# Performance work log

Hardware: AMD Instinct MI355X
Metric: run time of the kernel (lower is better)

The kernel has to match this reference:

```python
import jax, jax.numpy as jnp
import numpy as np
import math

B, S, D, H = 2, 2048, 1024, 16
DK = D // H


def setup_inputs() -> dict:
    key = jax.random.key(0)
    ks = jax.random.split(key, 11)
    f = jnp.float32
    return {
        "query": jax.random.normal(ks[0], (B, S, D), f),
        "key": jax.random.normal(ks[1], (B, S, D), f),
        "value": jax.random.normal(ks[2], (B, S, D), f),
        "wq": jax.random.normal(ks[3], (D, D), f) * 0.02,
        "bq": jnp.zeros((D,), f),
        "wk": jax.random.normal(ks[4], (D, D), f) * 0.02,
        "bk": jnp.zeros((D,), f),
        "wv": jax.random.normal(ks[5], (D, D), f) * 0.02,
        "bv": jnp.zeros((D,), f),
        "wo": jax.random.normal(ks[6], (D, D), f) * 0.02,
        "bo": jnp.zeros((D,), f),
    }


def reference(query, key, value, wq, bq, wk, bk, wv, bv, wo, bo):
    # Linear projections (torch Linear: y = x @ W.T + b)
    q = query @ wq.T + bq
    k = key @ wk.T + bk
    v = value @ wv.T + bv
    # [B,S,D] -> [B,H,S,DK]
    q = q.reshape(B, S, H, DK).transpose(0, 2, 1, 3)
    k = k.reshape(B, S, H, DK).transpose(0, 2, 1, 3)
    v = v.reshape(B, S, H, DK).transpose(0, 2, 1, 3)
    scores = jnp.einsum("bhqd,bhkd->bhqk", q, k) / math.sqrt(DK)
    causal = jnp.triu(jnp.ones((S, S), dtype=bool), k=1)  # strict upper triangle masked
    scores = jnp.where(causal, -jnp.inf, scores)
    attn = jax.nn.softmax(scores, axis=-1)  # dropout is identity in eval (p=0)
    x = jnp.einsum("bhqk,bhkd->bhqd", attn, v)
    x = x.transpose(0, 2, 1, 3).reshape(B, S, D)
    return x @ wo.T + bo
```

## Files before the change

### kernel.cpp

```cpp
#include <hip/hip_runtime.h>
#include <math.h>

#define BB 2
#define SS 2048
#define DD 1024
#define HH 16
#define DKK 64
#define MM (BB * SS)
#define KK DD
#define VSTR 2176

typedef __attribute__((ext_vector_type(8))) short short8;
typedef __attribute__((ext_vector_type(4))) float floatx4;

__device__ inline unsigned short f2bf(float x) {
    unsigned int u = __float_as_uint(x);
    u += 0x7fffu + ((u >> 16) & 1u);
    return (unsigned short)(u >> 16);
}

__device__ inline unsigned int pkbf(float a, float b) {
    return (__float_as_uint(b) & 0xffff0000u) | (__float_as_uint(a) >> 16);
}

__device__ inline void cast4f(const float* __restrict__ in, unsigned short* __restrict__ out, int i) {
    const float4 v = *(const float4*)(in + i);
    unsigned long long pk = (unsigned long long)f2bf(v.x)
                          | ((unsigned long long)f2bf(v.y) << 16)
                          | ((unsigned long long)f2bf(v.z) << 32)
                          | ((unsigned long long)f2bf(v.w) << 48);
    *(unsigned long long*)(out + i) = pk;
}

__global__ __launch_bounds__(256) void cast_all(const float* __restrict__ q, const float* __restrict__ k,
                                                const float* __restrict__ v,
                                                const float* __restrict__ wq, const float* __restrict__ wk,
                                                const float* __restrict__ wv, const float* __restrict__ wo,
                                                unsigned short* __restrict__ oq, unsigned short* __restrict__ ok,
                                                unsigned short* __restrict__ ov,
                                                unsigned short* __restrict__ owq, unsigned short* __restrict__ owk,
                                                unsigned short* __restrict__ owv, unsigned short* __restrict__ owo) {
    const int tid = blockIdx.x * 256 + threadIdx.x;
    #pragma unroll
    for (int it = 0; it < 8; ++it) {
        const int g = tid + it * 524288;
        const float* in;
        unsigned short* out;
        int idx;
        if (g < 3145728) {
            const int w = g >> 20;
            idx = g & 1048575;
            in  = (w == 0) ? q : (w == 1) ? k : v;
            out = (w == 0) ? oq : (w == 1) ? ok : ov;
        } else {
            const int gw = g - 3145728;
            const int w = gw >> 18;
            idx = gw & 262143;
            in  = (w == 0) ? wq : (w == 1) ? wk : (w == 2) ? wv : wo;
            out = (w == 0) ? owq : (w == 1) ? owk : (w == 2) ? owv : owo;
        }
        cast4f(in, out, idx * 4);
    }
}

#define GLDS(gp, lp) __builtin_amdgcn_global_load_lds( \
    (const __attribute__((address_space(1))) void*)(gp), \
    (__attribute__((address_space(3))) void*)(lp), 16, 0, 0)

#define SCHED0() __builtin_amdgcn_sched_barrier(0)
#define BAR()    __builtin_amdgcn_s_barrier()
#define WAITL0() asm volatile("s_waitcnt lgkmcnt(0)" ::: "memory")
#define WAITV(n) asm volatile("s_waitcnt vmcnt(" #n ")" ::: "memory")

__device__ __forceinline__ void gemm128_body(const unsigned short* __restrict__ A,
                                             const unsigned short* __restrict__ W,
                                             int m0, int n0,
                                             unsigned short* __restrict__ As,
                                             unsigned short* __restrict__ Bs,
                                             floatx4 (&acc)[4][4]) {
    const int t    = threadIdx.x;
    const int lane = t & 63;
    const int wave = t >> 6;
    const int col  = lane & 15;
    const int quad = lane >> 4;
    const int wm   = (wave >> 1) * 64;
    const int wn   = (wave & 1) * 64;

    const int r  = t >> 3;
    const int cs = t & 7;

    const int sA0 = (quad ^ (col & 7)) * 8;
    const int sA1 = ((quad + 4) ^ (col & 7)) * 8;

    auto stage = [&](int kt, int pb) {
        const int k0 = kt * 64;
        #pragma unroll
        for (int g = 0; g < 4; ++g) {
            const int row = g * 32 + r;
            const int ksw = (cs ^ (row & 7)) * 8;
            GLDS(A + (size_t)(m0 + row) * KK + k0 + ksw,
                 &As[pb * (128 * 64) + row * 64 + cs * 8]);
        }
        #pragma unroll
        for (int g = 0; g < 4; ++g) {
            const int row = g * 32 + r;
            const int ksw = (cs ^ (row & 7)) * 8;
            GLDS(W + (size_t)(n0 + row) * KK + k0 + ksw,
                 &Bs[pb * (128 * 64) + row * 64 + cs * 8]);
        }
    };

    stage(0, 0);
    WAITV(0); SCHED0(); BAR(); SCHED0();

    const int NK = KK / 64;
    for (int kt = 0; kt < NK; ++kt) {
        const int p = kt & 1;
        if (kt + 1 < NK) stage(kt + 1, p ^ 1);

        const unsigned short* Ab = &As[p * (128 * 64)];
        const unsigned short* Bb = &Bs[p * (128 * 64)];
        short8 a0[4], a1[4], b0[4], b1[4];
        #pragma unroll
        for (int i = 0; i < 4; ++i) {
            const unsigned short* ar = Ab + (wm + i * 16 + col) * 64;
            a0[i] = *(const short8*)(ar + sA0);
            a1[i] = *(const short8*)(ar + sA1);
        }
        #pragma unroll
        for (int j = 0; j < 4; ++j) {
            const unsigned short* br = Bb + (wn + j * 16 + col) * 64;
            b0[j] = *(const short8*)(br + sA0);
            b1[j] = *(const short8*)(br + sA1);
        }

        __builtin_amdgcn_s_setprio(1);
        #pragma unroll
        for (int i = 0; i < 4; ++i)
            #pragma unroll
            for (int j = 0; j < 4; ++j)
                acc[i][j] = __builtin_amdgcn_mfma_f32_16x16x32_bf16(a0[i], b0[j], acc[i][j], 0, 0, 0);
        #pragma unroll
        for (int i = 0; i < 4; ++i)
            #pragma unroll
            for (int j = 0; j < 4; ++j)
                acc[i][j] = __builtin_amdgcn_mfma_f32_16x16x32_bf16(a1[i], b1[j], acc[i][j], 0, 0, 0);
        __builtin_amdgcn_s_setprio(0);

        WAITL0(); SCHED0();
        if (kt + 1 < NK) { WAITV(0); }
        SCHED0(); BAR(); SCHED0();
    }
}

__global__ __launch_bounds__(256, 2) void gemm_qkv(const unsigned short* __restrict__ qB,
                                                   const unsigned short* __restrict__ kB,
                                                   const unsigned short* __restrict__ vB,
                                                   const unsigned short* __restrict__ wqB,
                                                   const unsigned short* __restrict__ wkB,
                                                   const unsigned short* __restrict__ wvB,
                                                   const float* __restrict__ bq,
                                                   const float* __restrict__ bk,
                                                   const float* __restrict__ bv,
                                                   unsigned short* __restrict__ Qh,
                                                   unsigned short* __restrict__ Kh,
                                                   unsigned short* __restrict__ Vt) {
    __shared__ __align__(16) unsigned short As[2 * 128 * 64];
    __shared__ __align__(16) unsigned short Bs[2 * 128 * 64];

    const int bid   = blockIdx.x;
    const int wgid  = (bid & 7) * 96 + (bid >> 3);
    const int which = wgid >> 8;
    const int tile  = wgid & 255;
    const int m0    = (tile >> 3) * 128;
    const int n0    = (tile & 7) * 128;

    const unsigned short* A = (which == 0) ? qB : (which == 1) ? kB : vB;
    const unsigned short* W = (which == 0) ? wqB : (which == 1) ? wkB : wvB;
    const float* bias       = (which == 0) ? bq : (which == 1) ? bk : bv;

    floatx4 acc[4][4] = {};
    gemm128_body(A, W, m0, n0, As, Bs, acc);

    const int t    = threadIdx.x;
    const int lane = t & 63;
    const int wave = t >> 6;
    const int col  = lane & 15;
    const int quad = lane >> 4;
    const int wm   = (wave >> 1) * 64;
    const int wn   = (wave & 1) * 64;

    #pragma unroll
    for (int i = 0; i < 4; ++i) {
        #pragma unroll
        for (int j = 0; j < 4; ++j) {
            const int n  = n0 + wn + j * 16 + col;
            const float bv0 = bias[n];
            const int h = n >> 6, dk = n & 63;
            const int mb  = m0 + wm + i * 16 + quad * 4;
            const int bdx = mb >> 11, s = mb & 2047;
            if (which != 2) {
                unsigned short* O = (which == 0) ? Qh : Kh;
                #pragma unroll
                for (int rr = 0; rr < 4; ++rr)
                    O[(((size_t)(bdx * HH + h)) * SS + (s + rr)) * DKK + dk] = f2bf(acc[i][j][rr] + bv0);
            } else {
                unsigned short* vp = Vt + (((size_t)(bdx * HH + h)) * DKK + dk) * VSTR + s;
                uint2 w;
                w.x = (unsigned int)f2bf(acc[i][j][0] + bv0) | ((unsigned int)f2bf(acc[i][j][1] + bv0) << 16);
                w.y = (unsigned int)f2bf(acc[i][j][2] + bv0) | ((unsigned int)f2bf(acc[i][j][3] + bv0) << 16);
                *(uint2*)vp = w;
            }
        }
    }
}

__global__ __launch_bounds__(256, 2) void gemm_out(const unsigned short* __restrict__ A,
                                                   const unsigned short* __restrict__ W,
                                                   const float* __restrict__ bias,
                                                   float* __restrict__ C) {
    __shared__ __align__(16) unsigned short As[2 * 128 * 64];
    __shared__ __align__(16) unsigned short Bs[2 * 128 * 64];

    const int bid  = blockIdx.x;
    const int wgid = (bid & 7) * 32 + (bid >> 3);
    const int m0   = (wgid >> 3) * 128;
    const int n0   = (wgid & 7) * 128;

    floatx4 acc[4][4] = {};
    gemm128_body(A, W, m0, n0, As, Bs, acc);

    const int t    = threadIdx.x;
    const int lane = t & 63;
    const int wave = t >> 6;
    const int col  = lane & 15;
    const int quad = lane >> 4;
    const int wm   = (wave >> 1) * 64;
    const int wn   = (wave & 1) * 64;

    #pragma unroll
    for (int i = 0; i < 4; ++i) {
        #pragma unroll
        for (int j = 0; j < 4; ++j) {
            const int n = n0 + wn + j * 16 + col;
            const float bv0 = bias[n];
            #pragma unroll
            for (int rr = 0; rr < 4; ++rr) {
                const int m = m0 + wm + i * 16 + quad * 4 + rr;
                C[(size_t)m * DD + n] = acc[i][j][rr] + bv0;
            }
        }
    }
}

#define C1 0.18033688011112042f
#define C2 11.541560327111707f
#define MFMA __builtin_amdgcn_mfma_f32_16x16x32_bf16

__global__ __launch_bounds__(512) void attn_mfma(const unsigned short* __restrict__ Qh,
                                                 const unsigned short* __restrict__ Kh,
                                                 const unsigned short* __restrict__ Vt,
                                                 unsigned short* __restrict__ X) {
    __shared__ __align__(16) unsigned short Ks[2][64 * 64];
    __shared__ __align__(16) unsigned short Vs[2][64 * 64];
    __shared__ __align__(16) unsigned short Plds[8][16 * 40];

    const int t    = threadIdx.x;
    const int lane = t & 63;
    const int wave = t >> 6;
    const int col  = lane & 15;
    const int quad = lane >> 4;

    const int lin = blockIdx.x;
    const int bh  = (lin & 7) + 8 * ((lin >> 3) & 3);
    const int pr  = lin >> 5;
    const int b   = bh / HH, h = bh % HH;

    const int cX  = (wave < 4) ? (31 - pr) : pr;
    const int q0  = cX * 64 + (wave & 3) * 16;
    const int nst = 32 - pr;

    const unsigned short* Kb = Kh + (size_t)bh * SS * DKK;
    const unsigned short* Vb = Vt + (size_t)bh * DKK * VSTR;

    const int r0  = t >> 3;
    const int sg0 = ((t & 7) ^ (r0 & 7)) * 8;

    unsigned short* Pw = &Plds[wave][0];

    const unsigned short* Qb = Qh + ((size_t)bh * SS + q0) * DKK;
    const short8 qa0 = *(const short8*)(Qb + (size_t)col * DKK + quad * 8);
    const short8 qa1 = *(const short8*)(Qb + (size_t)col * DKK + 32 + quad * 8);

    floatx4 o0 = {0.f, 0.f, 0.f, 0.f}, o1 = o0, o2 = o0, o3 = o0;
    float lp = 0.f;

    const int ksA = ((quad)      ^ (col & 7)) * 8;
    const int ksB = ((quad | 4)  ^ (col & 7)) * 8;

    GLDS(Kb + (size_t)r0 * DKK + sg0,  &Ks[0][t * 8]);
    GLDS(Vb + (size_t)r0 * VSTR + sg0, &Vs[0][t * 8]);

    int cur = 0;
    for (int kb = 0; kb < nst; ++kb) {
        __syncthreads();

        if (kb + 1 < nst) {
            const int jn = (kb + 1) * 64;
            const int nx = cur ^ 1;
            GLDS(Kb + (size_t)(jn + r0) * DKK + sg0,  &Ks[nx][t * 8]);
            GLDS(Vb + (size_t)r0 * VSTR + jn + sg0,   &Vs[nx][t * 8]);
        }

        const unsigned short* Kp = &Ks[cur][0];
        const unsigned short* Vp = &Vs[cur][0];

        #pragma unroll
        for (int hh = 0; hh < 2; ++hh) {
            const int j0 = kb * 64 + hh * 32;
            if (j0 < q0 + 16) {
                const short8 k0 = *(const short8*)(Kp + (hh * 32 + col) * 64 + ksA);
                const short8 k1 = *(const short8*)(Kp + (hh * 32 + col) * 64 + ksB);
                const short8 k2 = *(const short8*)(Kp + (hh * 32 + col + 16) * 64 + ksA);
                const short8 k3 = *(const short8*)(Kp + (hh * 32 + col + 16) * 64 + ksB);

                floatx4 t0 = {0.f, 0.f, 0.f, 0.f}, t1 = t0;
                __builtin_amdgcn_s_setprio(1);
                t0 = MFMA(k0, qa0, t0, 0, 0, 0);
                t0 = MFMA(k1, qa1, t0, 0, 0, 0);
                t1 = MFMA(k2, qa0, t1, 0, 0, 0);
                t1 = MFMA(k3, qa1, t1, 0, 0, 0);
                __builtin_amdgcn_s_setprio(0);

                float p[8];
                if (j0 + 31 > q0) {
                    const int lim = q0 + col - j0;
                    #pragma unroll
                    for (int r = 0; r < 4; ++r) {
                        p[r]     = (quad * 4 + r      <= lim) ? __builtin_exp2f(fmaf(t0[r], C1, -C2)) : 0.f;
                        p[4 + r] = (16 + quad * 4 + r <= lim) ? __builtin_exp2f(fmaf(t1[r], C1, -C2)) : 0.f;
                    }
                } else {
                    #pragma unroll
                    for (int r = 0; r < 4; ++r) {
                        p[r]     = __builtin_exp2f(fmaf(t0[r], C1, -C2));
                        p[4 + r] = __builtin_exp2f(fmaf(t1[r], C1, -C2));
                    }
                }
                lp += (p[0] + p[1]) + (p[2] + p[3]) + (p[4] + p[5]) + (p[6] + p[7]);

                uint2 w0 = { pkbf(p[0], p[1]), pkbf(p[2], p[3]) };
                uint2 w1 = { pkbf(p[4], p[5]), pkbf(p[6], p[7]) };
                *(uint2*)(Pw + col * 40 + quad * 4)      = w0;
                *(uint2*)(Pw + col * 40 + 16 + quad * 4) = w1;

                const short8 pb = *(const short8*)(Pw + col * 40 + quad * 8);
                const int vs = hh ? ksB : ksA;
                const short8 v0 = *(const short8*)(Vp + (col)      * 64 + vs);
                const short8 v1 = *(const short8*)(Vp + (col + 16) * 64 + vs);
                const short8 v2 = *(const short8*)(Vp + (col + 32) * 64 + vs);
                const short8 v3 = *(const short8*)(Vp + (col + 48) * 64 + vs);
                __builtin_amdgcn_s_setprio(1);
                o0 = MFMA(v0, pb, o0, 0, 0, 0);
                o1 = MFMA(v1, pb, o1, 0, 0, 0);
                o2 = MFMA(v2, pb, o2, 0, 0, 0);
                o3 = MFMA(v3, pb, o3, 0, 0, 0);
                __builtin_amdgcn_s_setprio(0);
            }
        }

        cur ^= 1;
    }

    lp += __shfl_xor(lp, 16, 64);
    lp += __shfl_xor(lp, 32, 64);
    const float li = 1.f / lp;

    unsigned short* Xp = X + ((size_t)(b * SS + q0 + col)) * DD + h * DKK + quad * 4;
    {
        uint2 w;
        w.x = (unsigned int)f2bf(o0[0] * li) | ((unsigned int)f2bf(o0[1] * li) << 16);
        w.y = (unsigned int)f2bf(o0[2] * li) | ((unsigned int)f2bf(o0[3] * li) << 16);
        *(uint2*)(Xp + 0) = w;
        w.x = (unsigned int)f2bf(o1[0] * li) | ((unsigned int)f2bf(o1[1] * li) << 16);
        w.y = (unsigned int)f2bf(o1[2] * li) | ((unsigned int)f2bf(o1[3] * li) << 16);
        *(uint2*)(Xp + 16) = w;
        w.x = (unsigned int)f2bf(o2[0] * li) | ((unsigned int)f2bf(o2[1] * li) << 16);
        w.y = (unsigned int)f2bf(o2[2] * li) | ((unsigned int)f2bf(o2[3] * li) << 16);
        *(uint2*)(Xp + 32) = w;
        w.x = (unsigned int)f2bf(o3[0] * li) | ((unsigned int)f2bf(o3[1] * li) << 16);
        w.y = (unsigned int)f2bf(o3[2] * li) | ((unsigned int)f2bf(o3[3] * li) << 16);
        *(uint2*)(Xp + 48) = w;
    }
}

extern "C" void kernel_launch(void* const* d_in, const int* in_sizes, int n_in,
                              void* d_out, int out_size, void* d_ws, size_t ws_size,
                              hipStream_t stream) {
    const float* query = (const float*)d_in[0];
    const float* key   = (const float*)d_in[1];
    const float* value = (const float*)d_in[2];
    const float* wq    = (const float*)d_in[3];
    const float* bq    = (const float*)d_in[4];
    const float* wk    = (const float*)d_in[5];
    const float* bk    = (const float*)d_in[6];
    const float* wv    = (const float*)d_in[7];
    const float* bv    = (const float*)d_in[8];
    const float* wo    = (const float*)d_in[9];
    const float* bo    = (const float*)d_in[10];

    char* ws = (char*)d_ws;
    const size_t MB = 1024 * 1024;
    unsigned short* qB  = (unsigned short*)(ws);
    unsigned short* kB  = (unsigned short*)(ws + 8 * MB);
    unsigned short* vB  = (unsigned short*)(ws + 16 * MB);
    unsigned short* wqB = (unsigned short*)(ws + 24 * MB);
    unsigned short* wkB = (unsigned short*)(ws + 26 * MB);
    unsigned short* wvB = (unsigned short*)(ws + 28 * MB);
    unsigned short* woB = (unsigned short*)(ws + 30 * MB);
    unsigned short* Qh  = (unsigned short*)(ws + 32 * MB);
    unsigned short* Kh  = (unsigned short*)(ws + 40 * MB);
    unsigned short* Vt  = (unsigned short*)(ws + 48 * MB);
    unsigned short* Xb  = qB;

    cast_all<<<2048, 256, 0, stream>>>(query, key, value, wq, wk, wv, wo,
                                       qB, kB, vB, wqB, wkB, wvB, woB);

    gemm_qkv<<<768, 256, 0, stream>>>(qB, kB, vB, wqB, wkB, wvB, bq, bk, bv, Qh, Kh, Vt);

    attn_mfma<<<512, 512, 0, stream>>>(Qh, Kh, Vt, Xb);

    gemm_out<<<256, 256, 0, stream>>>(Xb, woB, bo, (float*)d_out);
}
```

Before: 219.8 us.

## Fuse fp32-to-bf16 casts into GEMM tile loading, drop separate cast kernel

```diff
diff --git a/kernel.cpp b/kernel.cpp
--- a/kernel.cpp
+++ b/kernel.cpp
@@ -23,44 +23,19 @@
     return (__float_as_uint(b) & 0xffff0000u) | (__float_as_uint(a) >> 16);
 }
 
-__device__ inline void cast4f(const float* __restrict__ in, unsigned short* __restrict__ out, int i) {
-    const float4 v = *(const float4*)(in + i);
-    unsigned long long pk = (unsigned long long)f2bf(v.x)
-                          | ((unsigned long long)f2bf(v.y) << 16)
-                          | ((unsigned long long)f2bf(v.z) << 32)
-                          | ((unsigned long long)f2bf(v.w) << 48);
-    *(unsigned long long*)(out + i) = pk;
-}
-
-__global__ __launch_bounds__(256) void cast_all(const float* __restrict__ q, const float* __restrict__ k,
-                                                const float* __restrict__ v,
-                                                const float* __restrict__ wq, const float* __restrict__ wk,
-                                                const float* __restrict__ wv, const float* __restrict__ wo,
-                                                unsigned short* __restrict__ oq, unsigned short* __restrict__ ok,
-                                                unsigned short* __restrict__ ov,
-                                                unsigned short* __restrict__ owq, unsigned short* __restrict__ owk,
-                                                unsigned short* __restrict__ owv, unsigned short* __restrict__ owo) {
-    const int tid = blockIdx.x * 256 + threadIdx.x;
-    #pragma unroll
-    for (int it = 0; it < 8; ++it) {
-        const int g = tid + it * 524288;
-        const float* in;
-        unsigned short* out;
-        int idx;
-        if (g < 3145728) {
-            const int w = g >> 20;
-            idx = g & 1048575;
-            in  = (w == 0) ? q : (w == 1) ? k : v;
-            out = (w == 0) ? oq : (w == 1) ? ok : ov;
-        } else {
-            const int gw = g - 3145728;
-            const int w = gw >> 18;
-            idx = gw & 262143;
-            in  = (w == 0) ? wq : (w == 1) ? wk : (w == 2) ? wv : wo;
-            out = (w == 0) ? owq : (w == 1) ? owk : (w == 2) ? owv : owo;
-        }
-        cast4f(in, out, idx * 4);
-    }
+__device__ inline unsigned int rhu2(float a, float b) {
+    const unsigned int au = __float_as_uint(a) + 0x8000u;
+    const unsigned int bu = __float_as_uint(b) + 0x8000u;
+    return (bu & 0xffff0000u) | (au >> 16);
+}
+
+__device__ inline short8 pack8(const float4 x, const float4 y) {
+    union { unsigned int u[4]; short8 s; } r;
+    r.u[0] = rhu2(x.x, x.y);
+    r.u[1] = rhu2(x.z, x.w);
+    r.u[2] = rhu2(y.x, y.y);
+    r.u[3] = rhu2(y.z, y.w);
+    return r.s;
 }
 
 #define GLDS(gp, lp) __builtin_amdgcn_global_load_lds( \
@@ -72,93 +47,13 @@
 #define WAITL0() asm volatile("s_waitcnt lgkmcnt(0)" ::: "memory")
 #define WAITV(n) asm volatile("s_waitcnt vmcnt(" #n ")" ::: "memory")
 
-__device__ __forceinline__ void gemm128_body(const unsigned short* __restrict__ A,
-                                             const unsigned short* __restrict__ W,
-                                             int m0, int n0,
-                                             unsigned short* __restrict__ As,
-                                             unsigned short* __restrict__ Bs,
-                                             floatx4 (&acc)[4][4]) {
-    const int t    = threadIdx.x;
-    const int lane = t & 63;
-    const int wave = t >> 6;
-    const int col  = lane & 15;
-    const int quad = lane >> 4;
-    const int wm   = (wave >> 1) * 64;
-    const int wn   = (wave & 1) * 64;
-
-    const int r  = t >> 3;
-    const int cs = t & 7;
-
-    const int sA0 = (quad ^ (col & 7)) * 8;
-    const int sA1 = ((quad + 4) ^ (col & 7)) * 8;
-
-    auto stage = [&](int kt, int pb) {
-        const int k0 = kt * 64;
-        #pragma unroll
-        for (int g = 0; g < 4; ++g) {
-            const int row = g * 32 + r;
-            const int ksw = (cs ^ (row & 7)) * 8;
-            GLDS(A + (size_t)(m0 + row) * KK + k0 + ksw,
-                 &As[pb * (128 * 64) + row * 64 + cs * 8]);
-        }
-        #pragma unroll
-        for (int g = 0; g < 4; ++g) {
-            const int row = g * 32 + r;
-            const int ksw = (cs ^ (row & 7)) * 8;
-            GLDS(W + (size_t)(n0 + row) * KK + k0 + ksw,
-                 &Bs[pb * (128 * 64) + row * 64 + cs * 8]);
-        }
-    };
-
-    stage(0, 0);
-    WAITV(0); SCHED0(); BAR(); SCHED0();
-
-    const int NK = KK / 64;
-    for (int kt = 0; kt < NK; ++kt) {
-        const int p = kt & 1;
-        if (kt + 1 < NK) stage(kt + 1, p ^ 1);
-
-        const unsigned short* Ab = &As[p * (128 * 64)];
-        const unsigned short* Bb = &Bs[p * (128 * 64)];
-        short8 a0[4], a1[4], b0[4], b1[4];
-        #pragma unroll
-        for (int i = 0; i < 4; ++i) {
-            const unsigned short* ar = Ab + (wm + i * 16 + col) * 64;
-            a0[i] = *(const short8*)(ar + sA0);
-            a1[i] = *(const short8*)(ar + sA1);
-        }
-        #pragma unroll
-        for (int j = 0; j < 4; ++j) {
-            const unsigned short* br = Bb + (wn + j * 16 + col) * 64;
-            b0[j] = *(const short8*)(br + sA0);
-            b1[j] = *(const short8*)(br + sA1);
-        }
-
-        __builtin_amdgcn_s_setprio(1);
-        #pragma unroll
-        for (int i = 0; i < 4; ++i)
-            #pragma unroll
-            for (int j = 0; j < 4; ++j)
-                acc[i][j] = __builtin_amdgcn_mfma_f32_16x16x32_bf16(a0[i], b0[j], acc[i][j], 0, 0, 0);
-        #pragma unroll
-        for (int i = 0; i < 4; ++i)
-            #pragma unroll
-            for (int j = 0; j < 4; ++j)
-                acc[i][j] = __builtin_amdgcn_mfma_f32_16x16x32_bf16(a1[i], b1[j], acc[i][j], 0, 0, 0);
-        __builtin_amdgcn_s_setprio(0);
-
-        WAITL0(); SCHED0();
-        if (kt + 1 < NK) { WAITV(0); }
-        SCHED0(); BAR(); SCHED0();
-    }
-}
-
-__global__ __launch_bounds__(256, 2) void gemm_qkv(const unsigned short* __restrict__ qB,
-                                                   const unsigned short* __restrict__ kB,
-                                                   const unsigned short* __restrict__ vB,
-                                                   const unsigned short* __restrict__ wqB,
-                                                   const unsigned short* __restrict__ wkB,
-                                                   const unsigned short* __restrict__ wvB,
+
+__global__ __launch_bounds__(256, 2) void gemm_qkv(const float* __restrict__ q,
+                                                   const float* __restrict__ k,
+                                                   const float* __restrict__ v,
+                                                   const float* __restrict__ wq,
+                                                   const float* __restrict__ wk,
+                                                   const float* __restrict__ wv,
                                                    const float* __restrict__ bq,
                                                    const float* __restrict__ bk,
                                                    const float* __restrict__ bv,
@@ -175,12 +70,9 @@
     const int m0    = (tile >> 3) * 128;
     const int n0    = (tile & 7) * 128;
 
-    const unsigned short* A = (which == 0) ? qB : (which == 1) ? kB : vB;
-    const unsigned short* W = (which == 0) ? wqB : (which == 1) ? wkB : wvB;
-    const float* bias       = (which == 0) ? bq : (which == 1) ? bk : bv;
-
-    floatx4 acc[4][4] = {};
-    gemm128_body(A, W, m0, n0, As, Bs, acc);
+    const float* A    = (which == 0) ? q : (which == 1) ? k : v;
+    const float* W    = (which == 0) ? wq : (which == 1) ? wk : wv;
+    const float* bias = (which == 0) ? bq : (which == 1) ? bk : bv;
 
     const int t    = threadIdx.x;
     const int lane = t & 63;
@@ -189,6 +81,86 @@
     const int quad = lane >> 4;
     const int wm   = (wave >> 1) * 64;
     const int wn   = (wave & 1) * 64;
+
+    const int sr = t >> 1;
+    const int kh = t & 1;
+    const float* Ag = A + (size_t)(m0 + sr) * KK + kh * 32;
+    const float* Wg = W + (size_t)(n0 + sr) * KK + kh * 32;
+    int wof[4];
+    #pragma unroll
+    for (int j = 0; j < 4; ++j) wof[j] = sr * 64 + ((kh * 4 + j) ^ (sr & 7)) * 8;
+
+    const int sA0 = (quad ^ (col & 7)) * 8;
+    const int sA1 = ((quad + 4) ^ (col & 7)) * 8;
+
+    floatx4 acc[4][4] = {};
+    float4 la[8], lb[8];
+
+    #pragma unroll
+    for (int i = 0; i < 8; ++i) la[i] = *(const float4*)(Ag + i * 4);
+    #pragma unroll
+    for (int i = 0; i < 8; ++i) lb[i] = *(const float4*)(Wg + i * 4);
+    #pragma unroll
+    for (int j = 0; j < 4; ++j) *(short8*)(&As[wof[j]]) = pack8(la[2 * j], la[2 * j + 1]);
+    #pragma unroll
+    for (int j = 0; j < 4; ++j) *(short8*)(&Bs[wof[j]]) = pack8(lb[2 * j], lb[2 * j + 1]);
+    WAITL0(); SCHED0(); BAR(); SCHED0();
+
+    const int NK = KK / 64;
+    for (int kt = 0; kt < NK; ++kt) {
+        const int p = kt & 1;
+
+        if (kt + 1 < NK) {
+            const float* pa = Ag + (kt + 1) * 64;
+            const float* pw = Wg + (kt + 1) * 64;
+            #pragma unroll
+            for (int i = 0; i < 8; ++i) la[i] = *(const float4*)(pa + i * 4);
+            #pragma unroll
+            for (int i = 0; i < 8; ++i) lb[i] = *(const float4*)(pw + i * 4);
+        }
+        SCHED0();
+
+        const unsigned short* Ab = &As[p * (128 * 64)];
+        const unsigned short* Bb = &Bs[p * (128 * 64)];
+        short8 a0[4], a1[4], b0[4], b1[4];
+        #pragma unroll
+        for (int i = 0; i < 4; ++i) {
+            const unsigned short* ar = Ab + (wm + i * 16 + col) * 64;
+            a0[i] = *(const short8*)(ar + sA0);
+            a1[i] = *(const short8*)(ar + sA1);
+        }
+        #pragma unroll
+        for (int j = 0; j < 4; ++j) {
+            const unsigned short* br = Bb + (wn + j * 16 + col) * 64;
+            b0[j] = *(const short8*)(br + sA0);
+            b1[j] = *(const short8*)(br + sA1);
+        }
+
+        __builtin_amdgcn_s_setprio(1);
+        #pragma unroll
+        for (int i = 0; i < 4; ++i)
+            #pragma unroll
+            for (int j = 0; j < 4; ++j)
+                acc[i][j] = __builtin_amdgcn_mfma_f32_16x16x32_bf16(a0[i], b0[j], acc[i][j], 0, 0, 0);
+        #pragma unroll
+        for (int i = 0; i < 4; ++i)
+            #pragma unroll
+            for (int j = 0; j < 4; ++j)
+                acc[i][j] = __builtin_amdgcn_mfma_f32_16x16x32_bf16(a1[i], b1[j], acc[i][j], 0, 0, 0);
+        __builtin_amdgcn_s_setprio(0);
+
+        if (kt + 1 < NK) {
+            unsigned short* Ad = &As[(p ^ 1) * (128 * 64)];
+            unsigned short* Bd = &Bs[(p ^ 1) * (128 * 64)];
+            #pragma unroll
+            for (int j = 0; j < 4; ++j) *(short8*)(Ad + wof[j]) = pack8(la[2 * j], la[2 * j + 1]);
+            #pragma unroll
+            for (int j = 0; j < 4; ++j) *(short8*)(Bd + wof[j]) = pack8(lb[2 * j], lb[2 * j + 1]);
+        }
+
+        WAITL0(); SCHED0();
+        BAR(); SCHED0();
+    }
 
     #pragma unroll
     for (int i = 0; i < 4; ++i) {
@@ -216,7 +188,7 @@
 }
 
 __global__ __launch_bounds__(256, 2) void gemm_out(const unsigned short* __restrict__ A,
-                                                   const unsigned short* __restrict__ W,
+                                                   const float* __restrict__ W,
                                                    const float* __restrict__ bias,
                                                    float* __restrict__ C) {
     __shared__ __align__(16) unsigned short As[2 * 128 * 64];
@@ -226,9 +198,6 @@
     const int wgid = (bid & 7) * 32 + (bid >> 3);
     const int m0   = (wgid >> 3) * 128;
     const int n0   = (wgid & 7) * 128;
-
-    floatx4 acc[4][4] = {};
-    gemm128_body(A, W, m0, n0, As, Bs, acc);
 
     const int t    = threadIdx.x;
     const int lane = t & 63;
@@ -238,6 +207,92 @@
     const int wm   = (wave >> 1) * 64;
     const int wn   = (wave & 1) * 64;
 
+    const int r  = t >> 3;
+    const int cs = t & 7;
+
+    const int sr = t >> 1;
+    const int kh = t & 1;
+    const float* Wg = W + (size_t)(n0 + sr) * KK + kh * 32;
+    int wof[4];
+    #pragma unroll
+    for (int j = 0; j < 4; ++j) wof[j] = sr * 64 + ((kh * 4 + j) ^ (sr & 7)) * 8;
+
+    const int sA0 = (quad ^ (col & 7)) * 8;
+    const int sA1 = ((quad + 4) ^ (col & 7)) * 8;
+
+    auto stageA = [&](int kt, int pb) {
+        const int k0 = kt * 64;
+        #pragma unroll
+        for (int g = 0; g < 4; ++g) {
+            const int row = g * 32 + r;
+            const int ksw = (cs ^ (row & 7)) * 8;
+            GLDS(A + (size_t)(m0 + row) * KK + k0 + ksw,
+                 &As[pb * (128 * 64) + row * 64 + cs * 8]);
+        }
+    };
+
+    floatx4 acc[4][4] = {};
+    float4 lb[8];
+
+    stageA(0, 0);
+    #pragma unroll
+    for (int i = 0; i < 8; ++i) lb[i] = *(const float4*)(Wg + i * 4);
+    #pragma unroll
+    for (int j = 0; j < 4; ++j) *(short8*)(&Bs[wof[j]]) = pack8(lb[2 * j], lb[2 * j + 1]);
+    WAITL0(); WAITV(0); SCHED0(); BAR(); SCHED0();
+
+    const int NK = KK / 64;
+    for (int kt = 0; kt < NK; ++kt) {
+        const int p = kt & 1;
+
+        if (kt + 1 < NK) {
+            stageA(kt + 1, p ^ 1);
+            const float* pw = Wg + (kt + 1) * 64;
+            #pragma unroll
+            for (int i = 0; i < 8; ++i) lb[i] = *(const float4*)(pw + i * 4);
+        }
+        SCHED0();
+
+        const unsigned short* Ab = &As[p * (128 * 64)];
+        const unsigned short* Bb = &Bs[p * (128 * 64)];
+        short8 a0[4], a1[4], b0[4], b1[4];
+        #pragma unroll
+        for (int i = 0; i < 4; ++i) {
+            const unsigned short* ar = Ab + (wm + i * 16 + col) * 64;
+            a0[i] = *(const short8*)(ar + sA0);
+            a1[i] = *(const short8*)(ar + sA1);
+        }
+        #pragma unroll
+        for (int j = 0; j < 4; ++j) {
+            const unsigned short* br = Bb + (wn + j * 16 + col) * 64;
+            b0[j] = *(const short8*)(br + sA0);
+            b1[j] = *(const short8*)(br + sA1);
+        }
+
+        __builtin_amdgcn_s_setprio(1);
+        #pragma unroll
+        for (int i = 0; i < 4; ++i)
+            #pragma unroll
+            for (int j = 0; j < 4; ++j)
+                acc[i][j] = __builtin_amdgcn_mfma_f32_16x16x32_bf16(a0[i], b0[j], acc[i][j], 0, 0, 0);
+        #pragma unroll
+        for (int i = 0; i < 4; ++i)
+            #pragma unroll
+            for (int j = 0; j < 4; ++j)
+                acc[i][j] = __builtin_amdgcn_mfma_f32_16x16x32_bf16(a1[i], b1[j], acc[i][j], 0, 0, 0);
+        __builtin_amdgcn_s_setprio(0);
+
+        if (kt + 1 < NK) {
+            unsigned short* Bd = &Bs[(p ^ 1) * (128 * 64)];
+            #pragma unroll
+            for (int j = 0; j < 4; ++j) *(short8*)(Bd + wof[j]) = pack8(lb[2 * j], lb[2 * j + 1]);
+        }
+
+        WAITL0(); SCHED0();
+        if (kt + 1 < NK) { WAITV(0); }
+        SCHED0(); BAR(); SCHED0();
+    }
+
     #pragma unroll
     for (int i = 0; i < 4; ++i) {
         #pragma unroll
@@ -336,15 +391,15 @@
                 if (j0 + 31 > q0) {
                     const int lim = q0 + col - j0;
                     #pragma unroll
-                    for (int r = 0; r < 4; ++r) {
-                        p[r]     = (quad * 4 + r      <= lim) ? __builtin_exp2f(fmaf(t0[r], C1, -C2)) : 0.f;
-                        p[4 + r] = (16 + quad * 4 + r <= lim) ? __builtin_exp2f(fmaf(t1[r], C1, -C2)) : 0.f;
+                    for (int rr = 0; rr < 4; ++rr) {
+                        p[rr]     = (quad * 4 + rr      <= lim) ? __builtin_exp2f(fmaf(t0[rr], C1, -C2)) : 0.f;
+                        p[4 + rr] = (16 + quad * 4 + rr <= lim) ? __builtin_exp2f(fmaf(t1[rr], C1, -C2)) : 0.f;
                     }
                 } else {
                     #pragma unroll
-                    for (int r = 0; r < 4; ++r) {
-                        p[r]     = __builtin_exp2f(fmaf(t0[r], C1, -C2));
-                        p[4 + r] = __builtin_exp2f(fmaf(t1[r], C1, -C2));
+                    for (int rr = 0; rr < 4; ++rr) {
+                        p[rr]     = __builtin_exp2f(fmaf(t0[rr], C1, -C2));
+                        p[4 + rr] = __builtin_exp2f(fmaf(t1[rr], C1, -C2));
                     }
                 }
                 lp += (p[0] + p[1]) + (p[2] + p[3]) + (p[4] + p[5]) + (p[6] + p[7]);
@@ -411,24 +466,14 @@
 
     char* ws = (char*)d_ws;
     const size_t MB = 1024 * 1024;
-    unsigned short* qB  = (unsigned short*)(ws);
-    unsigned short* kB  = (unsigned short*)(ws + 8 * MB);
-    unsigned short* vB  = (unsigned short*)(ws + 16 * MB);
-    unsigned short* wqB = (unsigned short*)(ws + 24 * MB);
-    unsigned short* wkB = (unsigned short*)(ws + 26 * MB);
-    unsigned short* wvB = (unsigned short*)(ws + 28 * MB);
-    unsigned short* woB = (unsigned short*)(ws + 30 * MB);
-    unsigned short* Qh  = (unsigned short*)(ws + 32 * MB);
-    unsigned short* Kh  = (unsigned short*)(ws + 40 * MB);
-    unsigned short* Vt  = (unsigned short*)(ws + 48 * MB);
-    unsigned short* Xb  = qB;
-
-    cast_all<<<2048, 256, 0, stream>>>(query, key, value, wq, wk, wv, wo,
-                                       qB, kB, vB, wqB, wkB, wvB, woB);
-
-    gemm_qkv<<<768, 256, 0, stream>>>(qB, kB, vB, wqB, wkB, wvB, bq, bk, bv, Qh, Kh, Vt);
+    unsigned short* Qh = (unsigned short*)(ws);
+    unsigned short* Kh = (unsigned short*)(ws + 8 * MB);
+    unsigned short* Vt = (unsigned short*)(ws + 16 * MB);
+    unsigned short* Xb = (unsigned short*)(ws + 25 * MB);
+
+    gemm_qkv<<<768, 256, 0, stream>>>(query, key, value, wq, wk, wv, bq, bk, bv, Qh, Kh, Vt);
 
     attn_mfma<<<512, 512, 0, stream>>>(Qh, Kh, Vt, Xb);
 
-    gemm_out<<<256, 256, 0, stream>>>(Xb, woB, bo, (float*)d_out);
-}
+    gemm_out<<<256, 256, 0, stream>>>(Xb, wo, bo, (float*)d_out);
+}
```

New measurement: 295.6 us. 1.34x slower.

## Fuse cast, QKV GEMM, attention and output GEMM into one persistent kernel

Applied to the files above, without the earlier changes.

```diff
diff --git a/kernel.cpp b/kernel.cpp
--- a/kernel.cpp
+++ b/kernel.cpp
@@ -9,6 +9,7 @@
 #define MM (BB * SS)
 #define KK DD
 #define VSTR 2176
+#define NBLK 256
 
 typedef __attribute__((ext_vector_type(8))) short short8;
 typedef __attribute__((ext_vector_type(4))) float floatx4;
@@ -32,37 +33,6 @@
     *(unsigned long long*)(out + i) = pk;
 }
 
-__global__ __launch_bounds__(256) void cast_all(const float* __restrict__ q, const float* __restrict__ k,
-                                                const float* __restrict__ v,
-                                                const float* __restrict__ wq, const float* __restrict__ wk,
-                                                const float* __restrict__ wv, const float* __restrict__ wo,
-                                                unsigned short* __restrict__ oq, unsigned short* __restrict__ ok,
-                                                unsigned short* __restrict__ ov,
-                                                unsigned short* __restrict__ owq, unsigned short* __restrict__ owk,
-                                                unsigned short* __restrict__ owv, unsigned short* __restrict__ owo) {
-    const int tid = blockIdx.x * 256 + threadIdx.x;
-    #pragma unroll
-    for (int it = 0; it < 8; ++it) {
-        const int g = tid + it * 524288;
-        const float* in;
-        unsigned short* out;
-        int idx;
-        if (g < 3145728) {
-            const int w = g >> 20;
-            idx = g & 1048575;
-            in  = (w == 0) ? q : (w == 1) ? k : v;
-            out = (w == 0) ? oq : (w == 1) ? ok : ov;
-        } else {
-            const int gw = g - 3145728;
-            const int w = gw >> 18;
-            idx = gw & 262143;
-            in  = (w == 0) ? wq : (w == 1) ? wk : (w == 2) ? wv : wo;
-            out = (w == 0) ? owq : (w == 1) ? owk : (w == 2) ? owv : owo;
-        }
-        cast4f(in, out, idx * 4);
-    }
-}
-
 #define GLDS(gp, lp) __builtin_amdgcn_global_load_lds( \
     (const __attribute__((address_space(1))) void*)(gp), \
     (__attribute__((address_space(3))) void*)(lp), 16, 0, 0)
@@ -72,19 +42,31 @@
 #define WAITL0() asm volatile("s_waitcnt lgkmcnt(0)" ::: "memory")
 #define WAITV(n) asm volatile("s_waitcnt vmcnt(" #n ")" ::: "memory")
 
-__device__ __forceinline__ void gemm128_body(const unsigned short* __restrict__ A,
+__device__ inline void grid_sync(unsigned int* bar) {
+    __syncthreads();
+    if (threadIdx.x == 0) {
+        __threadfence();
+        const unsigned a = atomicAdd(&bar[0], 1u);
+        const unsigned target = ((a >> 8) + 1u) << 8;
+        while (atomicAdd(&bar[0], 0u) < target) __builtin_amdgcn_s_sleep(8);
+        __threadfence();
+    }
+    __syncthreads();
+}
+
+__device__ __forceinline__ void gemm512_body(const unsigned short* __restrict__ A,
                                              const unsigned short* __restrict__ W,
                                              int m0, int n0,
                                              unsigned short* __restrict__ As,
                                              unsigned short* __restrict__ Bs,
-                                             floatx4 (&acc)[4][4]) {
+                                             floatx4 (&acc)[4][2]) {
     const int t    = threadIdx.x;
     const int lane = t & 63;
     const int wave = t >> 6;
     const int col  = lane & 15;
     const int quad = lane >> 4;
-    const int wm   = (wave >> 1) * 64;
-    const int wn   = (wave & 1) * 64;
+    const int wm   = (wave >> 2) * 64;
+    const int wn   = (wave & 3) * 32;
 
     const int r  = t >> 3;
     const int cs = t & 7;
@@ -95,15 +77,15 @@
     auto stage = [&](int kt, int pb) {
         const int k0 = kt * 64;
         #pragma unroll
-        for (int g = 0; g < 4; ++g) {
-            const int row = g * 32 + r;
+        for (int g = 0; g < 2; ++g) {
+            const int row = g * 64 + r;
             const int ksw = (cs ^ (row & 7)) * 8;
             GLDS(A + (size_t)(m0 + row) * KK + k0 + ksw,
                  &As[pb * (128 * 64) + row * 64 + cs * 8]);
         }
         #pragma unroll
-        for (int g = 0; g < 4; ++g) {
-            const int row = g * 32 + r;
+        for (int g = 0; g < 2; ++g) {
+            const int row = g * 64 + r;
             const int ksw = (cs ^ (row & 7)) * 8;
             GLDS(W + (size_t)(n0 + row) * KK + k0 + ksw,
                  &Bs[pb * (128 * 64) + row * 64 + cs * 8]);
@@ -120,7 +102,7 @@
 
         const unsigned short* Ab = &As[p * (128 * 64)];
         const unsigned short* Bb = &Bs[p * (128 * 64)];
-        short8 a0[4], a1[4], b0[4], b1[4];
+        short8 a0[4], a1[4], b0[2], b1[2];
         #pragma unroll
         for (int i = 0; i < 4; ++i) {
             const unsigned short* ar = Ab + (wm + i * 16 + col) * 64;
@@ -128,7 +110,7 @@
             a1[i] = *(const short8*)(ar + sA1);
         }
         #pragma unroll
-        for (int j = 0; j < 4; ++j) {
+        for (int j = 0; j < 2; ++j) {
             const unsigned short* br = Bb + (wn + j * 16 + col) * 64;
             b0[j] = *(const short8*)(br + sA0);
             b1[j] = *(const short8*)(br + sA1);
@@ -138,12 +120,12 @@
         #pragma unroll
         for (int i = 0; i < 4; ++i)
             #pragma unroll
-            for (int j = 0; j < 4; ++j)
+            for (int j = 0; j < 2; ++j)
                 acc[i][j] = __builtin_amdgcn_mfma_f32_16x16x32_bf16(a0[i], b0[j], acc[i][j], 0, 0, 0);
         #pragma unroll
         for (int i = 0; i < 4; ++i)
             #pragma unroll
-            for (int j = 0; j < 4; ++j)
+            for (int j = 0; j < 2; ++j)
                 acc[i][j] = __builtin_amdgcn_mfma_f32_16x16x32_bf16(a1[i], b1[j], acc[i][j], 0, 0, 0);
         __builtin_amdgcn_s_setprio(0);
 
@@ -153,125 +135,25 @@
     }
 }
 
-__global__ __launch_bounds__(256, 2) void gemm_qkv(const unsigned short* __restrict__ qB,
-                                                   const unsigned short* __restrict__ kB,
-                                                   const unsigned short* __restrict__ vB,
-                                                   const unsigned short* __restrict__ wqB,
-                                                   const unsigned short* __restrict__ wkB,
-                                                   const unsigned short* __restrict__ wvB,
-                                                   const float* __restrict__ bq,
-                                                   const float* __restrict__ bk,
-                                                   const float* __restrict__ bv,
-                                                   unsigned short* __restrict__ Qh,
-                                                   unsigned short* __restrict__ Kh,
-                                                   unsigned short* __restrict__ Vt) {
-    __shared__ __align__(16) unsigned short As[2 * 128 * 64];
-    __shared__ __align__(16) unsigned short Bs[2 * 128 * 64];
-
-    const int bid   = blockIdx.x;
-    const int wgid  = (bid & 7) * 96 + (bid >> 3);
-    const int which = wgid >> 8;
-    const int tile  = wgid & 255;
-    const int m0    = (tile >> 3) * 128;
-    const int n0    = (tile & 7) * 128;
-
-    const unsigned short* A = (which == 0) ? qB : (which == 1) ? kB : vB;
-    const unsigned short* W = (which == 0) ? wqB : (which == 1) ? wkB : wvB;
-    const float* bias       = (which == 0) ? bq : (which == 1) ? bk : bv;
-
-    floatx4 acc[4][4] = {};
-    gemm128_body(A, W, m0, n0, As, Bs, acc);
-
+#define C1 0.18033688011112042f
+#define C2 11.541560327111707f
+#define MFMA __builtin_amdgcn_mfma_f32_16x16x32_bf16
+
+__device__ __forceinline__ void attn_pair(int lin,
+                                          const unsigned short* __restrict__ Qh,
+                                          const unsigned short* __restrict__ Kh,
+                                          const unsigned short* __restrict__ Vt,
+                                          unsigned short* __restrict__ X,
+                                          unsigned short* __restrict__ KsB,
+                                          unsigned short* __restrict__ VsB,
+                                          unsigned short* __restrict__ Plds)
+{
     const int t    = threadIdx.x;
     const int lane = t & 63;
     const int wave = t >> 6;
     const int col  = lane & 15;
     const int quad = lane >> 4;
-    const int wm   = (wave >> 1) * 64;
-    const int wn   = (wave & 1) * 64;
-
-    #pragma unroll
-    for (int i = 0; i < 4; ++i) {
-        #pragma unroll
-        for (int j = 0; j < 4; ++j) {
-            const int n  = n0 + wn + j * 16 + col;
-            const float bv0 = bias[n];
-            const int h = n >> 6, dk = n & 63;
-            const int mb  = m0 + wm + i * 16 + quad * 4;
-            const int bdx = mb >> 11, s = mb & 2047;
-            if (which != 2) {
-                unsigned short* O = (which == 0) ? Qh : Kh;
-                #pragma unroll
-                for (int rr = 0; rr < 4; ++rr)
-                    O[(((size_t)(bdx * HH + h)) * SS + (s + rr)) * DKK + dk] = f2bf(acc[i][j][rr] + bv0);
-            } else {
-                unsigned short* vp = Vt + (((size_t)(bdx * HH + h)) * DKK + dk) * VSTR + s;
-                uint2 w;
-                w.x = (unsigned int)f2bf(acc[i][j][0] + bv0) | ((unsigned int)f2bf(acc[i][j][1] + bv0) << 16);
-                w.y = (unsigned int)f2bf(acc[i][j][2] + bv0) | ((unsigned int)f2bf(acc[i][j][3] + bv0) << 16);
-                *(uint2*)vp = w;
-            }
-        }
-    }
-}
-
-__global__ __launch_bounds__(256, 2) void gemm_out(const unsigned short* __restrict__ A,
-                                                   const unsigned short* __restrict__ W,
-                                                   const float* __restrict__ bias,
-                                                   float* __restrict__ C) {
-    __shared__ __align__(16) unsigned short As[2 * 128 * 64];
-    __shared__ __align__(16) unsigned short Bs[2 * 128 * 64];
-
-    const int bid  = blockIdx.x;
-    const int wgid = (bid & 7) * 32 + (bid >> 3);
-    const int m0   = (wgid >> 3) * 128;
-    const int n0   = (wgid & 7) * 128;
-
-    floatx4 acc[4][4] = {};
-    gemm128_body(A, W, m0, n0, As, Bs, acc);
-
-    const int t    = threadIdx.x;
-    const int lane = t & 63;
-    const int wave = t >> 6;
-    const int col  = lane & 15;
-    const int quad = lane >> 4;
-    const int wm   = (wave >> 1) * 64;
-    const int wn   = (wave & 1) * 64;
-
-    #pragma unroll
-    for (int i = 0; i < 4; ++i) {
-        #pragma unroll
-        for (int j = 0; j < 4; ++j) {
-            const int n = n0 + wn + j * 16 + col;
-            const float bv0 = bias[n];
-            #pragma unroll
-            for (int rr = 0; rr < 4; ++rr) {
-                const int m = m0 + wm + i * 16 + quad * 4 + rr;
-                C[(size_t)m * DD + n] = acc[i][j][rr] + bv0;
-            }
-        }
-    }
-}
-
-#define C1 0.18033688011112042f
-#define C2 11.541560327111707f
-#define MFMA __builtin_amdgcn_mfma_f32_16x16x32_bf16
-
-__global__ __launch_bounds__(512) void attn_mfma(const unsigned short* __restrict__ Qh,
-                                                 const unsigned short* __restrict__ Kh,
-                                                 const unsigned short* __restrict__ Vt,
-                                                 unsigned short* __restrict__ X) {
-    __shared__ __align__(16) unsigned short Ks[2][64 * 64];
-    __shared__ __align__(16) unsigned short Vs[2][64 * 64];
-    __shared__ __align__(16) unsigned short Plds[8][16 * 40];
-
-    const int t    = threadIdx.x;
-    const int lane = t & 63;
-    const int wave = t >> 6;
-    const int col  = lane & 15;
-    const int quad = lane >> 4;
-
-    const int lin = blockIdx.x;
+
     const int bh  = (lin & 7) + 8 * ((lin >> 3) & 3);
     const int pr  = lin >> 5;
     const int b   = bh / HH, h = bh % HH;
@@ -286,7 +168,7 @@
     const int r0  = t >> 3;
     const int sg0 = ((t & 7) ^ (r0 & 7)) * 8;
 
-    unsigned short* Pw = &Plds[wave][0];
+    unsigned short* Pw = Plds + wave * 640;
 
     const unsigned short* Qb = Qh + ((size_t)bh * SS + q0) * DKK;
     const short8 qa0 = *(const short8*)(Qb + (size_t)col * DKK + quad * 8);
@@ -298,8 +180,10 @@
     const int ksA = ((quad)      ^ (col & 7)) * 8;
     const int ksB = ((quad | 4)  ^ (col & 7)) * 8;
 
-    GLDS(Kb + (size_t)r0 * DKK + sg0,  &Ks[0][t * 8]);
-    GLDS(Vb + (size_t)r0 * VSTR + sg0, &Vs[0][t * 8]);
+    __syncthreads();
+
+    GLDS(Kb + (size_t)r0 * DKK + sg0,  &KsB[t * 8]);
+    GLDS(Vb + (size_t)r0 * VSTR + sg0, &VsB[t * 8]);
 
     int cur = 0;
     for (int kb = 0; kb < nst; ++kb) {
@@ -308,12 +192,12 @@
         if (kb + 1 < nst) {
             const int jn = (kb + 1) * 64;
             const int nx = cur ^ 1;
-            GLDS(Kb + (size_t)(jn + r0) * DKK + sg0,  &Ks[nx][t * 8]);
-            GLDS(Vb + (size_t)r0 * VSTR + jn + sg0,   &Vs[nx][t * 8]);
-        }
-
-        const unsigned short* Kp = &Ks[cur][0];
-        const unsigned short* Vp = &Vs[cur][0];
+            GLDS(Kb + (size_t)(jn + r0) * DKK + sg0,  &KsB[nx * 4096 + t * 8]);
+            GLDS(Vb + (size_t)r0 * VSTR + jn + sg0,   &VsB[nx * 4096 + t * 8]);
+        }
+
+        const unsigned short* Kp = &KsB[cur * 4096];
+        const unsigned short* Vp = &VsB[cur * 4096];
 
         #pragma unroll
         for (int hh = 0; hh < 2; ++hh) {
@@ -336,15 +220,15 @@
                 if (j0 + 31 > q0) {
                     const int lim = q0 + col - j0;
                     #pragma unroll
-                    for (int r = 0; r < 4; ++r) {
-                        p[r]     = (quad * 4 + r      <= lim) ? __builtin_exp2f(fmaf(t0[r], C1, -C2)) : 0.f;
-                        p[4 + r] = (16 + quad * 4 + r <= lim) ? __builtin_exp2f(fmaf(t1[r], C1, -C2)) : 0.f;
+                    for (int rr = 0; rr < 4; ++rr) {
+                        p[rr]     = (quad * 4 + rr      <= lim) ? __builtin_exp2f(fmaf(t0[rr], C1, -C2)) : 0.f;
+                        p[4 + rr] = (16 + quad * 4 + rr <= lim) ? __builtin_exp2f(fmaf(t1[rr], C1, -C2)) : 0.f;
                     }
                 } else {
                     #pragma unroll
-                    for (int r = 0; r < 4; ++r) {
-                        p[r]     = __builtin_exp2f(fmaf(t0[r], C1, -C2));
-                        p[4 + r] = __builtin_exp2f(fmaf(t1[r], C1, -C2));
+                    for (int rr = 0; rr < 4; ++rr) {
+                        p[rr]     = __builtin_exp2f(fmaf(t0[rr], C1, -C2));
+                        p[4 + rr] = __builtin_exp2f(fmaf(t1[rr], C1, -C2));
                     }
                 }
                 lp += (p[0] + p[1]) + (p[2] + p[3]) + (p[4] + p[5]) + (p[6] + p[7]);
@@ -394,6 +278,144 @@
     }
 }
 
+__global__ __launch_bounds__(512, 2) void mega(
+        const float* __restrict__ query, const float* __restrict__ key,
+        const float* __restrict__ value,
+        const float* __restrict__ wq, const float* __restrict__ bq,
+        const float* __restrict__ wk, const float* __restrict__ bk,
+        const float* __restrict__ wv, const float* __restrict__ bv,
+        const float* __restrict__ wo, const float* __restrict__ bo,
+        unsigned short* __restrict__ qB, unsigned short* __restrict__ kB,
+        unsigned short* __restrict__ vB,
+        unsigned short* __restrict__ wqB, unsigned short* __restrict__ wkB,
+        unsigned short* __restrict__ wvB, unsigned short* __restrict__ woB,
+        unsigned short* __restrict__ Qh, unsigned short* __restrict__ Kh,
+        unsigned short* __restrict__ Vt, unsigned short* __restrict__ Xb,
+        float* __restrict__ C, unsigned int* __restrict__ bar) {
+    __shared__ __align__(16) unsigned char smem[65536];
+    unsigned short* As = (unsigned short*)smem;
+    unsigned short* Bs = (unsigned short*)(smem + 32768);
+
+    const int bid  = blockIdx.x;
+    const int t    = threadIdx.x;
+    const int lane = t & 63;
+    const int wave = t >> 6;
+    const int col  = lane & 15;
+    const int quad = lane >> 4;
+
+    {
+        const int g0 = bid * 512 + t;
+        #pragma unroll
+        for (int it = 0; it < 32; ++it) {
+            const int g = g0 + it * 131072;
+            const float* in;
+            unsigned short* out;
+            int idx;
+            if (g < 3145728) {
+                const int w = g >> 20;
+                idx = g & 1048575;
+                in  = (w == 0) ? query : (w == 1) ? key : value;
+                out = (w == 0) ? qB : (w == 1) ? kB : vB;
+            } else {
+                const int gw = g - 3145728;
+                const int w = gw >> 18;
+                idx = gw & 262143;
+                in  = (w == 0) ? wq : (w == 1) ? wk : (w == 2) ? wv : wo;
+                out = (w == 0) ? wqB : (w == 1) ? wkB : (w == 2) ? wvB : woB;
+            }
+            cast4f(in, out, idx * 4);
+        }
+    }
+
+    grid_sync(bar);
+
+    {
+        const int wm = (wave >> 2) * 64;
+        const int wn = (wave & 3) * 32;
+        #pragma unroll 1
+        for (int it = 0; it < 3; ++it) {
+            const int wgid  = (bid & 7) * 96 + (bid >> 3) + it * 32;
+            const int which = wgid >> 8;
+            const int tile  = wgid & 255;
+            const int m0    = (tile >> 3) * 128;
+            const int n0    = (tile & 7) * 128;
+
+            const unsigned short* A = (which == 0) ? qB : (which == 1) ? kB : vB;
+            const unsigned short* W = (which == 0) ? wqB : (which == 1) ? wkB : wvB;
+            const float* bias       = (which == 0) ? bq : (which == 1) ? bk : bv;
+
+            floatx4 acc[4][2] = {};
+            gemm512_body(A, W, m0, n0, As, Bs, acc);
+
+            #pragma unroll
+            for (int i = 0; i < 4; ++i) {
+                #pragma unroll
+                for (int j = 0; j < 2; ++j) {
+                    const int n  = n0 + wn + j * 16 + col;
+                    const float bv0 = bias[n];
+                    const int h = n >> 6, dk = n & 63;
+                    const int mb  = m0 + wm + i * 16 + quad * 4;
+                    const int bdx = mb >> 11, s = mb & 2047;
+                    if (which != 2) {
+                        unsigned short* O = (which == 0) ? Qh : Kh;
+                        #pragma unroll
+                        for (int rr = 0; rr < 4; ++rr)
+                            O[(((size_t)(bdx * HH + h)) * SS + (s + rr)) * DKK + dk] = f2bf(acc[i][j][rr] + bv0);
+                    } else {
+                        unsigned short* vp = Vt + (((size_t)(bdx * HH + h)) * DKK + dk) * VSTR + s;
+                        uint2 w;
+                        w.x = (unsigned int)f2bf(acc[i][j][0] + bv0) | ((unsigned int)f2bf(acc[i][j][1] + bv0) << 16);
+                        w.y = (unsigned int)f2bf(acc[i][j][2] + bv0) | ((unsigned int)f2bf(acc[i][j][3] + bv0) << 16);
+                        *(uint2*)vp = w;
+                    }
+                }
+            }
+        }
+    }
+
+    grid_sync(bar);
+
+    {
+        unsigned short* KsB  = (unsigned short*)smem;
+        unsigned short* VsB  = (unsigned short*)(smem + 16384);
+        unsigned short* Plds = (unsigned short*)(smem + 32768);
+
+        const int pr1 = bid >> 5;
+        const int bhb = bid & 31;
+        attn_pair(pr1 * 32 + bhb,        Qh, Kh, Vt, Xb, KsB, VsB, Plds);
+        attn_pair((15 - pr1) * 32 + bhb, Qh, Kh, Vt, Xb, KsB, VsB, Plds);
+    }
+
+    grid_sync(bar);
+
+    {
+        const int wgid = (bid & 7) * 32 + (bid >> 3);
+        const int m0   = (wgid >> 3) * 128;
+        const int n0   = (wgid & 7) * 128;
+        const int wm   = (wave >> 2) * 64;
+        const int wn   = (wave & 3) * 32;
+
+        __syncthreads();
+
+        floatx4 acc[4][2] = {};
+        gemm512_body(Xb, woB, m0, n0, As, Bs, acc);
+
+        #pragma unroll
+        for (int i = 0; i < 4; ++i) {
+            #pragma unroll
+            for (int j = 0; j < 2; ++j) {
+                const int n = n0 + wn + j * 16 + col;
+                const float bv0 = bo[n];
+                #pragma unroll
+                for (int rr = 0; rr < 4; ++rr) {
+                    const int m = m0 + wm + i * 16 + quad * 4 + rr;
+                    C[(size_t)m * DD + n] = acc[i][j][rr] + bv0;
+                }
+            }
+        }
+    }
+}
+
 extern "C" void kernel_launch(void* const* d_in, const int* in_sizes, int n_in,
                               void* d_out, int out_size, void* d_ws, size_t ws_size,
                               hipStream_t stream) {
@@ -422,13 +444,11 @@
     unsigned short* Kh  = (unsigned short*)(ws + 40 * MB);
     unsigned short* Vt  = (unsigned short*)(ws + 48 * MB);
     unsigned short* Xb  = qB;
-
-    cast_all<<<2048, 256, 0, stream>>>(query, key, value, wq, wk, wv, wo,
-                                       qB, kB, vB, wqB, wkB, wvB, woB);
-
-    gemm_qkv<<<768, 256, 0, stream>>>(qB, kB, vB, wqB, wkB, wvB, bq, bk, bv, Qh, Kh, Vt);
-
-    attn_mfma<<<512, 512, 0, stream>>>(Qh, Kh, Vt, Xb);
-
-    gemm_out<<<256, 256, 0, stream>>>(Xb, woB, bo, (float*)d_out);
-}
+    unsigned int*   bar = (unsigned int*)(ws + 57 * MB - 4096);
+
+    hipMemsetAsync(bar, 0, 64, stream);
+
+    mega<<<NBLK, 512, 0, stream>>>(query, key, value, wq, bq, wk, bk, wv, bv, wo, bo,
+                                   qB, kB, vB, wqB, wkB, wvB, woB,
+                                   Qh, Kh, Vt, Xb, (float*)d_out, bar);
+}
```

New measurement: 299.8 us. 36.4% more time.
